# Kernel tuning notes

Hardware: AMD Instinct MI355X
Metric: run time of the kernel (lower is better)

The kernel has to match this reference:

```python
import jax, jax.numpy as jnp
import numpy as np

B, D_IN, D_H = 8192, 1024, 1024


def setup_inputs() -> dict:
    key = jax.random.key(0)
    ks = jax.random.split(key, 11)
    s_in = 1.0 / np.sqrt(D_IN)
    s_h = 1.0 / np.sqrt(D_H)
    return {
        "x": jax.random.normal(ks[0], (B, D_IN), jnp.float32),
        "h": jax.random.normal(ks[1], (B, D_H), jnp.float32),
        "Wiz": jax.random.normal(ks[2], (D_IN, D_H), jnp.float32) * s_in,
        "Uhz": jax.random.normal(ks[3], (D_H, D_H), jnp.float32) * s_h,
        "bz": jax.random.normal(ks[4], (D_H,), jnp.float32) * 0.01,
        "Wir": jax.random.normal(ks[5], (D_IN, D_H), jnp.float32) * s_in,
        "Uhr": jax.random.normal(ks[6], (D_H, D_H), jnp.float32) * s_h,
        "br": jax.random.normal(ks[7], (D_H,), jnp.float32) * 0.01,
        "Win": jax.random.normal(ks[8], (D_IN, D_H), jnp.float32) * s_in,
        "Uhn": jax.random.normal(ks[9], (D_H, D_H), jnp.float32) * s_h,
        "bn": jax.random.normal(ks[10], (D_H,), jnp.float32) * 0.01,
    }


def reference(x, h, Wiz, Uhz, bz, Wir, Uhr, br, Win, Uhn, bn):
    # Concatenate input-side weights into one GEMM for efficiency; math identical.
    Wi = jnp.concatenate([Wiz, Wir, Win], axis=1)          # [D_in, 3H]
    xz, xr, xn = jnp.split(x @ Wi, 3, axis=1)              # each [B, H]
    Uh = jnp.concatenate([Uhz, Uhr], axis=1)               # [H, 2H]
    hz, hr = jnp.split(h @ Uh, 2, axis=1)
    z = jax.nn.sigmoid(xz + hz + bz)
    r = jax.nn.sigmoid(xr + hr + br)
    # Faithful to source: (r * h) @ Uhn, and act1 (sigmoid) for n, not tanh.
    n = jax.nn.sigmoid(xn + (r * h) @ Uhn + bn)
    return (1.0 - z) * h + z * n
```

## Files before the change

kernel.cpp:

```cpp
#include <hip/hip_runtime.h>
#include <hip/hip_bf16.h>

typedef __attribute__((ext_vector_type(8))) short short8;
typedef __attribute__((ext_vector_type(4))) float f32x4;

#define DEV __device__ __forceinline__

DEV float bf2f(unsigned short u) {
    union { unsigned int i; float f; } v;
    v.i = ((unsigned int)u) << 16;
    return v.f;
}
DEV unsigned short f2bf(float f) {
    union { float f; unsigned int i; } v; v.f = f;
    unsigned int r = v.i + 0x7FFFu + ((v.i >> 16) & 1u);
    return (unsigned short)(r >> 16);
}
DEV float sigmoidf_(float x) {
    return 1.0f / (1.0f + __expf(-x));
}

__global__ void conv_xh(const float* __restrict__ x, const float* __restrict__ h,
                        unsigned short* __restrict__ xw, unsigned short* __restrict__ hw,
                        int n)
{
    int i = (blockIdx.x * blockDim.x + threadIdx.x) * 8;
    const float* src; unsigned short* dst; int off;
    if (i < n) { src = x; dst = xw; off = i; }
    else       { src = h; dst = hw; off = i - n; }
    float4 a = *(const float4*)(src + off);
    float4 b = *(const float4*)(src + off + 4);
    union { uint4 v; unsigned short s[8]; } o;
    o.s[0]=f2bf(a.x); o.s[1]=f2bf(a.y); o.s[2]=f2bf(a.z); o.s[3]=f2bf(a.w);
    o.s[4]=f2bf(b.x); o.s[5]=f2bf(b.y); o.s[6]=f2bf(b.z); o.s[7]=f2bf(b.w);
    *(uint4*)(dst + off) = o.v;
}

__global__ void tconv(const float* __restrict__ Wiz, const float* __restrict__ Uhz,
                      const float* __restrict__ Wir, const float* __restrict__ Uhr,
                      const float* __restrict__ Win, const float* __restrict__ Uhn,
                      unsigned short* __restrict__ B1t, unsigned short* __restrict__ B3t)
{
    __shared__ float lds[32][33];
    const float* src; unsigned short* dst;
    switch (blockIdx.z) {
        case 0: src=Wiz; dst=B1t;                            break;
        case 1: src=Uhz; dst=B1t + 1024;                     break;
        case 2: src=Wir; dst=B1t + (size_t)1024*2048;        break;
        case 3: src=Uhr; dst=B1t + (size_t)1024*2048 + 1024; break;
        case 4: src=Win; dst=B3t;                            break;
        default: src=Uhn; dst=B3t + 1024;                    break;
    }
    int k0 = blockIdx.x * 32, n0 = blockIdx.y * 32;
    int tx = threadIdx.x & 31, ty = threadIdx.x >> 5;
    #pragma unroll
    for (int i = 0; i < 4; i++)
        lds[ty + 8*i][tx] = src[(size_t)(k0 + ty + 8*i)*1024 + n0 + tx];
    __syncthreads();
    #pragma unroll
    for (int i = 0; i < 4; i++)
        dst[(size_t)(n0 + ty + 8*i)*2048 + k0 + tx] = f2bf(lds[tx][ty + 8*i]);
}

DEV void stage_band_A(char* smem, const unsigned short* A0, const unsigned short* A1,
                      int buf, int band, int ktile, int gm, int tid)
{
    const unsigned short* src = (ktile < 16) ? A0 : A1;
    int kofs = (ktile & 15) * 64;
    #pragma unroll
    for (int j = 0; j < 2; ++j) {
        int o  = tid * 16 + j * 8192;
        int rp = o >> 7;
        int k  = (o & 127) >> 1;
        int m  = ((rp >> 6) << 7) | (band << 6) | (rp & 63);
        const unsigned short* g = src + (size_t)(gm + m) * 1024 + kofs + k;
        __builtin_amdgcn_global_load_lds(
            (const __attribute__((address_space(1))) void*)g,
            (__attribute__((address_space(3))) void*)(smem + buf*32768 + band*16384 + o),
            16, 0, 0);
    }
}
DEV void stage_band_B(char* smem, const unsigned short* Bt,
                      int buf, int band, int ktile, int gn, int tid)
{
    #pragma unroll
    for (int j = 0; j < 2; ++j) {
        int o  = tid * 16 + j * 8192;
        int rp = o >> 7;
        int k  = (o & 127) >> 1;
        int n  = ((rp >> 5) << 6) | (band << 5) | (rp & 31);
        const unsigned short* g = Bt + (size_t)(gn + n) * 2048 + ktile * 64 + k;
        __builtin_amdgcn_global_load_lds(
            (const __attribute__((address_space(1))) void*)g,
            (__attribute__((address_space(3))) void*)(smem + 65536 + buf*32768 + band*16384 + o),
            16, 0, 0);
    }
}

#define LOAD_A(BUF,MH)                                                        \
    { _Pragma("unroll") for (int mi = 0; mi < 4; mi++)                        \
      { _Pragma("unroll") for (int ks = 0; ks < 2; ks++)                      \
        af[mi][ks] = *(const short8*)(smem + (BUF)*32768 + (MH)*16384         \
                                      + abase + mi*2048 + ks*64); } }
#define LOAD_B(BUF,NH,DST)                                                    \
    { _Pragma("unroll") for (int ni = 0; ni < 2; ni++)                        \
      { _Pragma("unroll") for (int ks = 0; ks < 2; ks++)                      \
        DST[ni][ks] = *(const short8*)(smem + (BUF)*32768 + (NH)*16384        \
                                       + bbase + ni*2048 + ks*64); } }
#define MM(MH,NH,BF)                                                          \
    { _Pragma("unroll") for (int mi = 0; mi < 4; mi++)                        \
      { _Pragma("unroll") for (int ni = 0; ni < 2; ni++)                      \
        { _Pragma("unroll") for (int ks = 0; ks < 2; ks++)                    \
          acc[(MH)*4+mi][(NH)*2+ni] = __builtin_amdgcn_mfma_f32_16x16x32_bf16(\
              af[mi][ks], BF[ni][ks], acc[(MH)*4+mi][(NH)*2+ni], 0, 0, 0); } } }
#define PH_MID(DO_VM)                                                         \
    if (DO_VM) asm volatile("s_waitcnt vmcnt(6)" ::: "memory");               \
    __builtin_amdgcn_s_barrier();                                             \
    asm volatile("s_waitcnt lgkmcnt(0)" ::: "memory");                        \
    __builtin_amdgcn_s_setprio(1);
#define PH_END                                                                \
    __builtin_amdgcn_s_setprio(0);                                            \
    __builtin_amdgcn_s_barrier();

__global__ __launch_bounds__(512, 2)
void gemm1_8ph(const unsigned short* __restrict__ A0,
               const unsigned short* __restrict__ A1,
               const unsigned short* __restrict__ Bt,
               const float* __restrict__ bz, const float* __restrict__ br,
               const float* __restrict__ hsrc,
               float* __restrict__ zbuf, unsigned short* __restrict__ rh)
{
    extern __shared__ char smem[];
    const int tid = threadIdx.x;

    int wg = (blockIdx.x & 7) * 32 + (blockIdx.x >> 3);
    const int gm = (wg & 31) * 256;
    const int gn = (wg >> 5) * 256;

    const int w  = tid >> 6, l = tid & 63;
    const int wr = w >> 2, wc = w & 3;
    const int lr = l & 15, lk = l >> 4;

    const int abase = wr*8192 + lr*128 + lk*16;
    const int bbase = 65536 + wc*4096 + lr*128 + lk*16;

    f32x4 acc[8][4] = {};
    short8 af[4][2], bf0[2][2], bf1[2][2];

    stage_band_A(smem, A0, A1, 0, 0, 0, gm, tid);
    stage_band_A(smem, A0, A1, 0, 1, 0, gm, tid);
    stage_band_B(smem, Bt, 0, 0, 0, gn, tid);
    stage_band_B(smem, Bt, 0, 1, 0, gn, tid);
    stage_band_A(smem, A0, A1, 1, 0, 1, gm, tid);
    stage_band_B(smem, Bt, 1, 0, 1, gn, tid);
    stage_band_B(smem, Bt, 1, 1, 1, gn, tid);
    asm volatile("s_waitcnt vmcnt(6)" ::: "memory");
    __builtin_amdgcn_s_barrier();

    for (int it = 0; it < 16; ++it) {
        const int T  = 2 * it;
        const int t1 = (T+1 < 31) ? T+1 : 31;
        const int t2 = (T+2 < 31) ? T+2 : 31;
        const int t3 = (T+3 < 31) ? T+3 : 31;

        LOAD_A(0,0); LOAD_B(0,0,bf0);
        stage_band_A(smem, A0, A1, 1, 1, t1, gm, tid);
        PH_MID(false); MM(0,0,bf0); PH_END;
        LOAD_B(0,1,bf1);
        stage_band_A(smem, A0, A1, 0, 0, t2, gm, tid);
        PH_MID(false); MM(0,1,bf1); PH_END;
        LOAD_A(0,1);
        stage_band_B(smem, Bt, 0, 0, t2, gn, tid);
        PH_MID(false); MM(1,0,bf0); PH_END;
        stage_band_B(smem, Bt, 0, 1, t2, gn, tid);
        PH_MID(true); MM(1,1,bf1); PH_END;

        LOAD_A(1,0); LOAD_B(1,0,bf0);
        stage_band_A(smem, A0, A1, 0, 1, t2, gm, tid);
        PH_MID(false); MM(0,0,bf0); PH_END;
        LOAD_B(1,1,bf1);
        stage_band_A(smem, A0, A1, 1, 0, t3, gm, tid);
        PH_MID(false); MM(0,1,bf1); PH_END;
        LOAD_A(1,1);
        stage_band_B(smem, Bt, 1, 0, t3, gn, tid);
        PH_MID(false); MM(1,0,bf0); PH_END;
        stage_band_B(smem, Bt, 1, 1, t3, gn, tid);
        PH_MID(true); MM(1,1,bf1); PH_END;
    }

    #pragma unroll
    for (int Mi = 0; Mi < 8; Mi++) {
        #pragma unroll
        for (int j = 0; j < 4; j++) {
            int row = gm + wr*128 + Mi*16 + lk*4 + j;
            #pragma unroll
            for (int Ni = 0; Ni < 4; Ni++) {
                int col = gn + wc*64 + Ni*16 + lr;
                float v = acc[Mi][Ni][j];
                if (col < 1024) {
                    zbuf[(size_t)row*1024 + col] = sigmoidf_(v + bz[col]);
                } else {
                    int c = col - 1024;
                    float rv = sigmoidf_(v + br[c]);
                    rh[(size_t)row*1024 + c] = f2bf(rv * hsrc[(size_t)row*1024 + c]);
                }
            }
        }
    }
}

__global__ __launch_bounds__(256, 2)
void gemm2_m97(const unsigned short* __restrict__ A0,
               const unsigned short* __restrict__ A1,
               const unsigned short* __restrict__ Bt,
               const float* __restrict__ bn,
               const float* __restrict__ hsrc,
               const float* __restrict__ zbuf,
               float* __restrict__ out)
{
    __shared__ unsigned short lA[128*32];
    __shared__ unsigned short lB[128*32];
    const int tid = threadIdx.x;
    const int gm = blockIdx.x * 128, gn = blockIdx.y * 128;

    const int w  = tid >> 6, l = tid & 63;
    const int wm = (w >> 1) * 64, wn = (w & 1) * 64;
    const int lr = l & 15, lk = l >> 4;

    f32x4 acc[4][4] = {};

    const int srow = tid >> 2;
    const int scol = (tid & 3) * 8;
    char* lAp = (char*)lA + tid * 16;
    char* lBp = (char*)lB + tid * 16;

    for (int kt = 0; kt < 2048; kt += 32) {
        const unsigned short* Ab = (kt < 1024 ? A0 : A1)
                                 + (size_t)(gm + srow) * 1024 + (kt & 1023) + scol;
        const unsigned short* Bb = Bt + (size_t)(gn + srow) * 2048 + kt + scol;
        __syncthreads();
        __builtin_amdgcn_global_load_lds(
            (const __attribute__((address_space(1))) void*)Ab,
            (__attribute__((address_space(3))) void*)lAp, 16, 0, 0);
        __builtin_amdgcn_global_load_lds(
            (const __attribute__((address_space(1))) void*)(Ab + (size_t)64*1024),
            (__attribute__((address_space(3))) void*)(lAp + 4096), 16, 0, 0);
        __builtin_amdgcn_global_load_lds(
            (const __attribute__((address_space(1))) void*)Bb,
            (__attribute__((address_space(3))) void*)lBp, 16, 0, 0);
        __builtin_amdgcn_global_load_lds(
            (const __attribute__((address_space(1))) void*)(Bb + (size_t)64*2048),
            (__attribute__((address_space(3))) void*)(lBp + 4096), 16, 0, 0);
        __syncthreads();

        short8 af[4], bfr[4];
        #pragma unroll
        for (int mi = 0; mi < 4; mi++)
            af[mi] = *(const short8*)&lA[(wm + mi*16 + lr)*32 + lk*8];
        #pragma unroll
        for (int ni = 0; ni < 4; ni++)
            bfr[ni] = *(const short8*)&lB[(wn + ni*16 + lr)*32 + lk*8];
        #pragma unroll
        for (int mi = 0; mi < 4; mi++)
            #pragma unroll
            for (int ni = 0; ni < 4; ni++)
                acc[mi][ni] = __builtin_amdgcn_mfma_f32_16x16x32_bf16(
                    af[mi], bfr[ni], acc[mi][ni], 0, 0, 0);
    }

    #pragma unroll
    for (int mi = 0; mi < 4; mi++) {
        #pragma unroll
        for (int j = 0; j < 4; j++) {
            int row = gm + wm + mi*16 + lk*4 + j;
            #pragma unroll
            for (int ni = 0; ni < 4; ni++) {
                int col = gn + wn + ni*16 + lr;
                float nv = sigmoidf_(acc[mi][ni][j] + bn[col]);
                float zv = zbuf[(size_t)row*1024 + col];
                float hv = hsrc[(size_t)row*1024 + col];
                out[(size_t)row*1024 + col] = (1.0f - zv)*hv + zv*nv;
            }
        }
    }
}

extern "C" void kernel_launch(void* const* d_in, const int* in_sizes, int n_in,
                              void* d_out, int out_size, void* d_ws, size_t ws_size,
                              hipStream_t stream)
{
    const float* x   = (const float*)d_in[0];
    const float* h   = (const float*)d_in[1];
    const float* Wiz = (const float*)d_in[2];
    const float* Uhz = (const float*)d_in[3];
    const float* bz  = (const float*)d_in[4];
    const float* Wir = (const float*)d_in[5];
    const float* Uhr = (const float*)d_in[6];
    const float* br  = (const float*)d_in[7];
    const float* Win = (const float*)d_in[8];
    const float* Uhn = (const float*)d_in[9];
    const float* bn  = (const float*)d_in[10];
    float* out = (float*)d_out;

    char* ws = (char*)d_ws;
    const size_t MB = 1024ull * 1024ull;
    unsigned short* xw   = (unsigned short*)(ws + 0);
    unsigned short* hw   = (unsigned short*)(ws + 16*MB);
    unsigned short* B1t  = (unsigned short*)(ws + 32*MB);
    unsigned short* B3t  = (unsigned short*)(ws + 40*MB);
    float*          zbuf = (float*)(ws + 44*MB);
    unsigned short* rh   = (unsigned short*)(ws + 76*MB);

    const int B = 8192, H = 1024;

    (void)hipFuncSetAttribute((const void*)gemm1_8ph,
                              hipFuncAttributeMaxDynamicSharedMemorySize, 131072);

    conv_xh<<<dim3(2*B*H/8/256), dim3(256), 0, stream>>>(x, h, xw, hw, B*H);

    tconv<<<dim3(32, 32, 6), dim3(256), 0, stream>>>(
        Wiz, Uhz, Wir, Uhr, Win, Uhn, B1t, B3t);

    gemm1_8ph<<<dim3(256), dim3(512), 131072, stream>>>(
        xw, hw, B1t, bz, br, h, zbuf, rh);

    gemm2_m97<<<dim3(64, 8), dim3(256), 0, stream>>>(
        xw, rh, B3t, bn, h, zbuf, out);
}
```

Before: 312.3 us.

## Swizzle LDS tiles in gemm1 and remap blocks to XCD-local tile groups

The global-to-LDS staging now XOR-swizzles the 16-byte k-chunk position by row, and the fragment loads from LDS apply the matching swizzle. This is meant to remove bank conflicts on the 128-byte-stride LDS reads. The block-to-tile mapping is also changed so each XCD gets a contiguous 8x4 group of output tiles, which should improve L2 reuse of A and B rows. The cost is a little extra index arithmetic, and the change depends on the swizzle being identical on the write and read sides.

```diff
diff --git a/kernel.cpp b/kernel.cpp
--- a/kernel.cpp
+++ b/kernel.cpp
@@ -69,11 +69,11 @@
     int kofs = (ktile & 15) * 64;
     #pragma unroll
     for (int j = 0; j < 2; ++j) {
-        int o  = tid * 16 + j * 8192;
-        int rp = o >> 7;
-        int k  = (o & 127) >> 1;
-        int m  = ((rp >> 6) << 7) | (band << 6) | (rp & 63);
-        const unsigned short* g = src + (size_t)(gm + m) * 1024 + kofs + k;
+        int o   = tid * 16 + j * 8192;
+        int rp  = o >> 7;
+        int kel = (((o >> 4) & 7) ^ (rp & 7)) << 3;
+        int m   = ((rp >> 6) << 7) | (band << 6) | (rp & 63);
+        const unsigned short* g = src + (size_t)(gm + m) * 1024 + kofs + kel;
         __builtin_amdgcn_global_load_lds(
             (const __attribute__((address_space(1))) void*)g,
             (__attribute__((address_space(3))) void*)(smem + buf*32768 + band*16384 + o),
@@ -85,11 +85,11 @@
 {
     #pragma unroll
     for (int j = 0; j < 2; ++j) {
-        int o  = tid * 16 + j * 8192;
-        int rp = o >> 7;
-        int k  = (o & 127) >> 1;
-        int n  = ((rp >> 5) << 6) | (band << 5) | (rp & 31);
-        const unsigned short* g = Bt + (size_t)(gn + n) * 2048 + ktile * 64 + k;
+        int o   = tid * 16 + j * 8192;
+        int rp  = o >> 7;
+        int kel = (((o >> 4) & 7) ^ (rp & 7)) << 3;
+        int n   = ((rp >> 5) << 6) | (band << 5) | (rp & 31);
+        const unsigned short* g = Bt + (size_t)(gn + n) * 2048 + ktile * 64 + kel;
         __builtin_amdgcn_global_load_lds(
             (const __attribute__((address_space(1))) void*)g,
             (__attribute__((address_space(3))) void*)(smem + 65536 + buf*32768 + band*16384 + o),
@@ -101,12 +101,12 @@
     { _Pragma("unroll") for (int mi = 0; mi < 4; mi++)                        \
       { _Pragma("unroll") for (int ks = 0; ks < 2; ks++)                      \
         af[mi][ks] = *(const short8*)(smem + (BUF)*32768 + (MH)*16384         \
-                                      + abase + mi*2048 + ks*64); } }
+                        + arow + mi*2048 + ((((ks<<2)|lk)<<4) ^ aswz)); } }
 #define LOAD_B(BUF,NH,DST)                                                    \
     { _Pragma("unroll") for (int ni = 0; ni < 2; ni++)                        \
       { _Pragma("unroll") for (int ks = 0; ks < 2; ks++)                      \
         DST[ni][ks] = *(const short8*)(smem + (BUF)*32768 + (NH)*16384        \
-                                       + bbase + ni*2048 + ks*64); } }
+                        + brow + ni*2048 + ((((ks<<2)|lk)<<4) ^ aswz)); } }
 #define MM(MH,NH,BF)                                                          \
     { _Pragma("unroll") for (int mi = 0; mi < 4; mi++)                        \
       { _Pragma("unroll") for (int ni = 0; ni < 2; ni++)                      \
@@ -133,16 +133,19 @@
     extern __shared__ char smem[];
     const int tid = threadIdx.x;
 
-    int wg = (blockIdx.x & 7) * 32 + (blockIdx.x >> 3);
-    const int gm = (wg & 31) * 256;
-    const int gn = (wg >> 5) * 256;
+    const int bid = blockIdx.x;
+    const int xcd = bid & 7, j = bid >> 3;
+    const int mt  = (xcd >> 1) * 8 + (j >> 2);
+    const int nt  = (xcd & 1) * 4 + (j & 3);
+    const int gm = mt * 256, gn = nt * 256;
 
     const int w  = tid >> 6, l = tid & 63;
     const int wr = w >> 2, wc = w & 3;
     const int lr = l & 15, lk = l >> 4;
 
-    const int abase = wr*8192 + lr*128 + lk*16;
-    const int bbase = 65536 + wc*4096 + lr*128 + lk*16;
+    const int arow = wr*8192 + lr*128;
+    const int brow = 65536 + wc*4096 + lr*128;
+    const int aswz = (lr & 7) << 4;
 
     f32x4 acc[8][4] = {};
     short8 af[4][2], bf0[2][2], bf1[2][2];
@@ -166,24 +169,30 @@
         LOAD_A(0,0); LOAD_B(0,0,bf0);
         stage_band_A(smem, A0, A1, 1, 1, t1, gm, tid);
         PH_MID(false); MM(0,0,bf0); PH_END;
+
         LOAD_B(0,1,bf1);
         stage_band_A(smem, A0, A1, 0, 0, t2, gm, tid);
         PH_MID(false); MM(0,1,bf1); PH_END;
+
         LOAD_A(0,1);
         stage_band_B(smem, Bt, 0, 0, t2, gn, tid);
         PH_MID(false); MM(1,0,bf0); PH_END;
+
         stage_band_B(smem, Bt, 0, 1, t2, gn, tid);
         PH_MID(true); MM(1,1,bf1); PH_END;
 
         LOAD_A(1,0); LOAD_B(1,0,bf0);
         stage_band_A(smem, A0, A1, 0, 1, t2, gm, tid);
         PH_MID(false); MM(0,0,bf0); PH_END;
+
         LOAD_B(1,1,bf1);
         stage_band_A(smem, A0, A1, 1, 0, t3, gm, tid);
         PH_MID(false); MM(0,1,bf1); PH_END;
+
         LOAD_A(1,1);
         stage_band_B(smem, Bt, 1, 0, t3, gn, tid);
         PH_MID(false); MM(1,0,bf0); PH_END;
+
         stage_band_B(smem, Bt, 1, 1, t3, gn, tid);
         PH_MID(true); MM(1,1,bf1); PH_END;
     }
@@ -191,12 +200,12 @@
     #pragma unroll
     for (int Mi = 0; Mi < 8; Mi++) {
         #pragma unroll
-        for (int j = 0; j < 4; j++) {
-            int row = gm + wr*128 + Mi*16 + lk*4 + j;
+        for (int jj = 0; jj < 4; jj++) {
+            int row = gm + wr*128 + Mi*16 + lk*4 + jj;
             #pragma unroll
             for (int Ni = 0; Ni < 4; Ni++) {
                 int col = gn + wc*64 + Ni*16 + lr;
-                float v = acc[Mi][Ni][j];
+                float v = acc[Mi][Ni][jj];
                 if (col < 1024) {
                     zbuf[(size_t)row*1024 + col] = sigmoidf_(v + bz[col]);
                 } else {
```

Measured after the change: 296.0 us. 5.2% less time.
